# Optimization experiments

Measured on AMD Instinct MI355X. Metric: run time of the kernel, lower is better.

## Reference

```python
import jax, jax.numpy as jnp
import numpy as np

P = 2          # feature power
K = 128        # top-k neighbors
ALPHA = 1.0
BETA = 1.0
EPS = 1e-12


def _smooth_rank_l2(v):
    # v: [B, r]. torch: relu(-(v[:,None,:] - v[:,:,None])).sum(-1)
    # element [b,i,j] of diff = v[b,j] - v[b,i]; relu(-diff) = relu(v[b,i]-v[b,j])
    return jnp.sum(jax.nn.relu(v[:, :, None] - v[:, None, :]), axis=-1)  # [B, r]


def setup_inputs() -> dict:
    key = jax.random.key(0)
    k1, k2, k3 = jax.random.split(key, 3)
    B, d, N0 = 256, 2048, 7936
    return {
        "f_s": jax.random.normal(k1, (B, d), dtype=jnp.float32),
        "f_t": jax.random.normal(k2, (B, d), dtype=jnp.float32),
        "gallery": jax.random.normal(k3, (N0, d), dtype=jnp.float32),
    }


def reference(f_s, f_t, gallery):
    # pool='all': x.pow(p).view(B, -1)
    fs = f_s ** P                      # [B, d]
    ft = f_t ** P                      # [B, d]
    # statistics=True, layer 0: teacher_features = concat(existing, f_t)
    gal = jnp.concatenate([gallery, ft], axis=0)   # [N, d]

    d2 = (jnp.sum(ft * ft, axis=-1, keepdims=True)
          + jnp.sum(gal * gal, axis=-1)[None, :]
          - 2.0 * ft @ gal.T)                       # [B, N]
    tt_dist = jnp.sqrt(jnp.clip(d2, EPS, None))

    # k smallest distances (torch.sort ascending + slice [:k])
    neg_top, top_k_index = jax.lax.top_k(-tt_dist, K)
    t_value = -neg_top                               # [B, K], ascending

    # per-row re-gather of gallery and student-to-gallery distances
    gal_k = gal[top_k_index]                         # [B, K, d]
    s_d2 = (jnp.sum(fs * fs, axis=-1)[:, None]
            + jnp.sum(gal_k * gal_k, axis=-1)
            - 2.0 * jnp.einsum('bd,bkd->bk', fs, gal_k))
    s_value = jnp.sqrt(jnp.clip(s_d2, EPS, None))    # [B, K]

    main_loss = ALPHA * jnp.mean(jnp.abs(s_value[:, 0] - t_value[:, 0]))

    r = K - 1
    t_rank = _smooth_rank_l2(t_value[:, 1:])         # [B, r]
    s_rank = _smooth_rank_l2(s_value[:, 1:])         # [B, r]
    extra_loss = BETA * jnp.mean(jnp.linalg.norm(t_rank - s_rank, axis=1)) / r

    return main_loss + extra_loss
```

## Files before the change

### kernel.cpp

```cpp
#include <hip/hip_runtime.h>
#include <hip/hip_bf16.h>

#define BDIM 256
#define DDIM 2048
#define NGAL 7936
#define NTOT 8192
#define TOPK 128
#define EPSC 1e-12f

typedef __attribute__((ext_vector_type(8))) short bf16x8;
typedef __attribute__((ext_vector_type(4))) float f32x4;
typedef unsigned long long u64;

__device__ __forceinline__ short bfr(float x) {
  unsigned u = __float_as_uint(x);
  unsigned r = (u + 0x7FFFu + ((u >> 16) & 1u)) >> 16;
  return (short)r;
}

__global__ __launch_bounds__(256) void k_prep_gal(
    const float* __restrict__ f_t, const float* __restrict__ f_s,
    const float* __restrict__ gallery, short* __restrict__ Abf,
    short* __restrict__ Bbf, float* __restrict__ normA,
    float* __restrict__ galnorm) {
  int bx = blockIdx.x, t = threadIdx.x;
  int lane = t & 63, wv = t >> 6;
  if (bx < NGAL / 4) {
    int row = bx * 4 + wv;
    const float4* g4 = (const float4*)(gallery + (size_t)row * DDIM);
    float s = 0.f;
    for (int i = lane; i < DDIM / 4; i += 64) {
      float4 v = g4[i];
      *(short4*)&Bbf[(size_t)row * DDIM + i * 4] =
          make_short4(bfr(v.x), bfr(v.y), bfr(v.z), bfr(v.w));
      s += v.x * v.x + v.y * v.y + v.z * v.z + v.w * v.w;
    }
    for (int off = 32; off; off >>= 1) s += __shfl_xor(s, off);
    if (lane == 0) galnorm[row] = s;
    return;
  }
  int b = bx - NGAL / 4;
  const float4* t4 = (const float4*)(f_t + (size_t)b * DDIM);
  const float4* s4 = (const float4*)(f_s + (size_t)b * DDIM);
  float st = 0.f, ss = 0.f;
  for (int i = t; i < DDIM / 4; i += 256) {
    float4 v = t4[i];
    float4 q = make_float4(v.x * v.x, v.y * v.y, v.z * v.z, v.w * v.w);
    short4 qb = make_short4(bfr(q.x), bfr(q.y), bfr(q.z), bfr(q.w));
    *(short4*)&Abf[(size_t)b * DDIM + i * 4] = qb;
    *(short4*)&Bbf[(size_t)(NGAL + b) * DDIM + i * 4] = qb;
    st += q.x * q.x + q.y * q.y + q.z * q.z + q.w * q.w;
    float4 u_ = s4[i];
    float4 r = make_float4(u_.x * u_.x, u_.y * u_.y, u_.z * u_.z, u_.w * u_.w);
    *(short4*)&Abf[(size_t)(BDIM + b) * DDIM + i * 4] =
        make_short4(bfr(r.x), bfr(r.y), bfr(r.z), bfr(r.w));
    ss += r.x * r.x + r.y * r.y + r.z * r.z + r.w * r.w;
  }
  for (int off = 32; off; off >>= 1) {
    st += __shfl_xor(st, off);
    ss += __shfl_xor(ss, off);
  }
  __shared__ float red[8];
  if (lane == 0) { red[wv] = st; red[4 + wv] = ss; }
  __syncthreads();
  if (t == 0) {
    float a = red[0] + red[1] + red[2] + red[3];
    float c = red[4] + red[5] + red[6] + red[7];
    normA[b] = a;
    galnorm[NGAL + b] = a;
    normA[BDIM + b] = c;
  }
}

__global__ __launch_bounds__(256) void k_gemm(
    const short* __restrict__ Abf, const short* __restrict__ Bbf,
    const float* __restrict__ normA, const float* __restrict__ galnorm,
    float* __restrict__ d2) {
  __shared__ short S[2][12288];
  int t = threadIdx.x;
  int n0 = blockIdx.x * 128, m0 = blockIdx.y * 64;
  int lane = t & 63, wid = t >> 6;
  int wm = wid >> 1, wn = wid & 1;

  const short* gb[6];
  int lof[6];
#pragma unroll
  for (int q = 0; q < 6; ++q) {
    int c = t + q * 256;
    int r, j;
    const short* base;
    if (c < 512) {
      r = c >> 3; j = c & 7;
      base = Abf + (size_t)(m0 + r) * DDIM;
    } else {
      int cb = c - 512;
      r = cb >> 3; j = cb & 7;
      base = Bbf + (size_t)(n0 + r) * DDIM;
    }
    gb[q] = base + ((j * 8) ^ ((r & 7) << 3));
    lof[q] = c * 8;
  }

  int fr = lane & 15, fk = (lane >> 4) * 8;
  int axor = (fr & 7) << 3;
  f32x4 acc[2][4] = {};

#define STAGE(buf, kt)                                                       \
  {                                                                          \
    _Pragma("unroll") for (int q = 0; q < 6; ++q)                            \
        __builtin_amdgcn_global_load_lds(                                    \
            (const __attribute__((address_space(1))) void*)(gb[q] + (kt)),   \
            (__attribute__((address_space(3))) void*)(&S[buf][lof[q]]), 16,  \
            0, 0);                                                           \
  }

  STAGE(0, 0);
  __syncthreads();
  int cur = 0;
  for (int it = 0; it < DDIM / 64; ++it) {
    if (it + 1 < DDIM / 64) STAGE(cur ^ 1, (it + 1) * 64);
#pragma unroll
    for (int ks = 0; ks < 2; ++ks) {
      int ko = (ks * 32 + fk) ^ axor;
      bf16x8 av[2], bv[4];
#pragma unroll
      for (int mi = 0; mi < 2; ++mi)
        av[mi] = *(const bf16x8*)&S[cur][(wm * 32 + mi * 16 + fr) * 64 + ko];
#pragma unroll
      for (int ni = 0; ni < 4; ++ni)
        bv[ni] =
            *(const bf16x8*)&S[cur][4096 + (wn * 64 + ni * 16 + fr) * 64 + ko];
#pragma unroll
      for (int mi = 0; mi < 2; ++mi)
#pragma unroll
        for (int ni = 0; ni < 4; ++ni)
          acc[mi][ni] = __builtin_amdgcn_mfma_f32_16x16x32_bf16(
              av[mi], bv[ni], acc[mi][ni], 0, 0, 0);
    }
    __syncthreads();
    cur ^= 1;
  }
  int rrow = (lane >> 4) * 4;
#pragma unroll
  for (int mi = 0; mi < 2; ++mi) {
#pragma unroll
    for (int r = 0; r < 4; ++r) {
      int m = m0 + wm * 32 + mi * 16 + rrow + r;
      float nm = normA[m];
#pragma unroll
      for (int ni = 0; ni < 4; ++ni) {
        int n = n0 + wn * 64 + ni * 16 + fr;
        float v = nm + galnorm[n] - 2.0f * acc[mi][ni][r];
        v = fmaxf(v, EPSC);
        if (m < BDIM && n == NGAL + m) v = EPSC;
        d2[(size_t)m * NTOT + n] = v;
      }
    }
  }
#undef STAGE
}

__global__ __launch_bounds__(256) void k_part(
    const float* __restrict__ d2, u64* __restrict__ cand) {
  __shared__ unsigned rowu[2048];
  __shared__ unsigned hist[2][2048];
  __shared__ unsigned wsum[4];
  __shared__ u64 s_pref;
  __shared__ unsigned s_kneed, s_cnt;
  int c = blockIdx.x, b = blockIdx.y, t = threadIdx.x;
  int lane = t & 63, w = t >> 6;
  const uint4* src = (const uint4*)(d2 + (size_t)b * NTOT + c * 2048);
  ((uint4*)rowu)[t] = src[t];
  ((uint4*)rowu)[t + 256] = src[t + 256];
  if (t == 0) { s_pref = 0; s_kneed = TOPK; s_cnt = 0; }
#pragma unroll 1
  for (int p = 0; p < 4; ++p) {
    int sh = 33 - 11 * p;
    for (int i = t; i < 4096; i += 256) (&hist[0][0])[i] = 0;
    __syncthreads();
    u64 pref = s_pref;
    unsigned kn = s_kneed;
#pragma unroll
    for (int s = 0; s < 8; ++s) {
      int i = t + s * 256;
      u64 key = ((u64)rowu[i] << 11) | (unsigned)i;
      if ((key >> (sh + 11)) == pref) {
        unsigned bin = (unsigned)(key >> sh) & 2047u;
        unsigned slot = ((bin & 7u) << 8) | (bin >> 3);
        atomicAdd(&hist[w & 1][slot], 1u);
      }
    }
    __syncthreads();
    unsigned ls = 0;
#pragma unroll
    for (int q = 0; q < 8; ++q)
      ls += hist[0][q * 256 + t] + hist[1][q * 256 + t];
    unsigned incl = ls;
    for (int off = 1; off < 64; off <<= 1) {
      unsigned x = __shfl_up(incl, off);
      if (lane >= off) incl += x;
    }
    if (lane == 63) wsum[w] = incl;
    __syncthreads();
    unsigned woff = 0;
    for (int ww = 0; ww < w; ++ww) woff += wsum[ww];
    incl += woff;
    unsigned excl = incl - ls;
    if (excl < kn && kn <= incl) {
      unsigned re = excl, binj = 0;
      for (int q = 0; q < 8; ++q) {
        unsigned h = hist[0][q * 256 + t] + hist[1][q * 256 + t];
        if (kn <= re + h) { binj = ((unsigned)t << 3) | (unsigned)q; break; }
        re += h;
      }
      s_pref = (pref << 11) | binj;
      s_kneed = kn - re;
    }
    __syncthreads();
  }
  u64 kstar = s_pref;
  u64* dst = cand + ((size_t)b * 4 + c) * TOPK;
#pragma unroll 1
  for (int s = 0; s < 8; ++s) {
    int i = t + s * 256;
    unsigned u = rowu[i];
    u64 key = ((u64)u << 11) | (unsigned)i;
    bool pred = (key <= kstar);
    u64 mask = __ballot(pred);
    unsigned base;
    if (lane == 0) base = atomicAdd(&s_cnt, (unsigned)__popcll(mask));
    base = (unsigned)__shfl((int)base, 0);
    if (pred) {
      unsigned pos = base + (unsigned)__popcll(mask & ((1ull << lane) - 1));
      dst[pos] = ((u64)u << 13) | (unsigned)(c * 2048 + i);
    }
  }
}

__global__ __launch_bounds__(256) void k_mloss(
    const u64* __restrict__ cand, const float* __restrict__ d2,
    float* __restrict__ out) {
  __shared__ u64 sk[512];
  __shared__ float tvs[TOPK], svs[TOPK], red[2];
  int b = blockIdx.x, t = threadIdx.x;
  u64 k0 = cand[(size_t)b * 512 + t];
  u64 k1 = cand[(size_t)b * 512 + 256 + t];
  sk[t] = k0;
  sk[t + 256] = k1;
  __syncthreads();
  int r0 = 0, r1 = 0;
  for (int j = 0; j < 512; ++j) {
    u64 kj = sk[j];
    r0 += (kj < k0);
    r1 += (kj < k1);
  }
  const float* srow = d2 + (size_t)(BDIM + b) * NTOT;
  if (r0 < TOPK) {
    tvs[r0] = sqrtf(__uint_as_float((unsigned)(k0 >> 13)));
    svs[r0] = sqrtf(srow[(unsigned)(k0 & 8191u)]);
  }
  if (r1 < TOPK) {
    tvs[r1] = sqrtf(__uint_as_float((unsigned)(k1 >> 13)));
    svs[r1] = sqrtf(srow[(unsigned)(k1 & 8191u)]);
  }
  __syncthreads();
  float val = 0.f;
  if (t >= 1 && t < TOPK) {
    float tv = tvs[t], sv = svs[t];
    float tr = 0.f, sr = 0.f;
    for (int j = 0; j < TOPK; ++j) {
      tr += fmaxf(tv - tvs[j], 0.f);
      sr += fmaxf(sv - svs[j], 0.f);
    }
    tr -= fmaxf(tv - tvs[0], 0.f);
    sr -= fmaxf(sv - svs[0], 0.f);
    float d = tr - sr;
    val = d * d;
  }
  int lane = t & 63, w = t >> 6;
  for (int off = 1; off < 64; off <<= 1) val += __shfl_xor(val, off);
  if (lane == 0) red[w] = val;
  __syncthreads();
  if (t == 0) {
    float sum = red[0] + red[1];
    float contrib = (1.f / 256.f) * fabsf(svs[0] - tvs[0]) +
                    (1.f / (127.f * 256.f)) * sqrtf(sum);
    atomicAdd(out, contrib);
  }
}

extern "C" void kernel_launch(void* const* d_in, const int* in_sizes, int n_in,
                              void* d_out, int out_size, void* d_ws,
                              size_t ws_size, hipStream_t stream) {
  const float* f_s = (const float*)d_in[0];
  const float* f_t = (const float*)d_in[1];
  const float* gallery = (const float*)d_in[2];
  float* out = (float*)d_out;

  float* d2 = (float*)d_ws;
  short* Abf = (short*)(d2 + (size_t)512 * NTOT);
  short* Bbf = Abf + (size_t)512 * DDIM;
  float* normA = (float*)(Bbf + (size_t)NTOT * DDIM);
  float* galnorm = normA + 512;
  u64* cand = (u64*)(galnorm + NTOT);

  hipMemsetAsync(d_out, 0, sizeof(float), stream);

  k_prep_gal<<<NGAL / 4 + BDIM, 256, 0, stream>>>(f_t, f_s, gallery, Abf, Bbf,
                                                  normA, galnorm);
  k_gemm<<<dim3(NTOT / 128, 512 / 64), 256, 0, stream>>>(Abf, Bbf, normA,
                                                         galnorm, d2);
  k_part<<<dim3(4, BDIM), 256, 0, stream>>>(d2, cand);
  k_mloss<<<BDIM, 256, 0, stream>>>(cand, d2, out);
}
```

Baseline: 163.2 us.

## Swizzle GEMM tiles per XCD and cut radix-select passes to three

The GEMM launch becomes a 1D grid whose block index is remapped so that consecutive blocks on each XCD share N tiles and all 8 M tiles. This is meant to raise L2 reuse of the gallery operand. The top-k partition kernel now radix-selects on the 32-bit value alone in three passes (11/11/10 bits) instead of four passes on a 43-bit value+index key, and breaks ties among equal values with a small index-rank pass. This removes one histogram pass and the 64-bit key arithmetic, at the cost of extra tie-handling logic that caps equal-value collection at 256 entries.

```diff
diff --git a/kernel.cpp b/kernel.cpp
--- a/kernel.cpp
+++ b/kernel.cpp
@@ -78,7 +78,11 @@
     float* __restrict__ d2) {
   __shared__ short S[2][12288];
   int t = threadIdx.x;
-  int n0 = blockIdx.x * 128, m0 = blockIdx.y * 64;
+  int swz = blockIdx.x;
+  int xcd = swz & 7, p = swz >> 3;
+  int nt = xcd * 8 + (p >> 3);
+  int mt = p & 7;
+  int n0 = nt * 128, m0 = mt * 64;
   int lane = t & 63, wid = t >> 6;
   int wm = wid >> 1, wn = wid & 1;
 
@@ -165,27 +169,32 @@
   __shared__ unsigned rowu[2048];
   __shared__ unsigned hist[2][2048];
   __shared__ unsigned wsum[4];
-  __shared__ u64 s_pref;
-  __shared__ unsigned s_kneed, s_cnt;
+  __shared__ unsigned s_pref, s_kneed, s_cnt, s_eqcnt;
+  __shared__ unsigned short eqidx[256];
   int c = blockIdx.x, b = blockIdx.y, t = threadIdx.x;
   int lane = t & 63, w = t >> 6;
   const uint4* src = (const uint4*)(d2 + (size_t)b * NTOT + c * 2048);
   ((uint4*)rowu)[t] = src[t];
   ((uint4*)rowu)[t + 256] = src[t + 256];
-  if (t == 0) { s_pref = 0; s_kneed = TOPK; s_cnt = 0; }
+  if (t == 0) { s_pref = 0; s_kneed = TOPK; s_cnt = 0; s_eqcnt = 0; }
 #pragma unroll 1
-  for (int p = 0; p < 4; ++p) {
-    int sh = 33 - 11 * p;
-    for (int i = t; i < 4096; i += 256) (&hist[0][0])[i] = 0;
-    __syncthreads();
-    u64 pref = s_pref;
-    unsigned kn = s_kneed;
+  for (int p = 0; p < 3; ++p) {
+    int sh = (p == 0) ? 21 : (p == 1) ? 10 : 0;
+    uint4 z4 = make_uint4(0, 0, 0, 0);
+    ((uint4*)&hist[0][0])[t] = z4;
+    ((uint4*)&hist[0][0])[t + 256] = z4;
+    ((uint4*)&hist[0][0])[t + 512] = z4;
+    ((uint4*)&hist[0][0])[t + 768] = z4;
+    __syncthreads();
+    unsigned pref = s_pref, kn = s_kneed;
+    int sh_hi = (p == 1) ? 21 : 10;
+    unsigned bmask = (p == 2) ? 1023u : 2047u;
 #pragma unroll
     for (int s = 0; s < 8; ++s) {
-      int i = t + s * 256;
-      u64 key = ((u64)rowu[i] << 11) | (unsigned)i;
-      if ((key >> (sh + 11)) == pref) {
-        unsigned bin = (unsigned)(key >> sh) & 2047u;
+      unsigned u = rowu[t + s * 256];
+      bool sel = (p == 0) || ((u >> sh_hi) == pref);
+      if (sel) {
+        unsigned bin = (u >> sh) & bmask;
         unsigned slot = ((bin & 7u) << 8) | (bin >> 3);
         atomicAdd(&hist[w & 1][slot], 1u);
       }
@@ -213,26 +222,43 @@
         if (kn <= re + h) { binj = ((unsigned)t << 3) | (unsigned)q; break; }
         re += h;
       }
-      s_pref = (pref << 11) | binj;
+      unsigned bits = (p == 2) ? 10u : 11u;
+      s_pref = (pref << bits) | binj;
       s_kneed = kn - re;
     }
     __syncthreads();
   }
-  u64 kstar = s_pref;
+  unsigned vstar = s_pref;
+  unsigned kneed = s_kneed;
   u64* dst = cand + ((size_t)b * 4 + c) * TOPK;
 #pragma unroll 1
   for (int s = 0; s < 8; ++s) {
     int i = t + s * 256;
     unsigned u = rowu[i];
-    u64 key = ((u64)u << 11) | (unsigned)i;
-    bool pred = (key <= kstar);
-    u64 mask = __ballot(pred);
-    unsigned base;
-    if (lane == 0) base = atomicAdd(&s_cnt, (unsigned)__popcll(mask));
-    base = (unsigned)__shfl((int)base, 0);
-    if (pred) {
-      unsigned pos = base + (unsigned)__popcll(mask & ((1ull << lane) - 1));
+    bool lt = (u < vstar);
+    u64 mlt = __ballot(lt);
+    unsigned basep;
+    if (lane == 0) basep = atomicAdd(&s_cnt, (unsigned)__popcll(mlt));
+    basep = (unsigned)__shfl((int)basep, 0);
+    if (lt) {
+      unsigned pos = basep + (unsigned)__popcll(mlt & ((1ull << lane) - 1));
       dst[pos] = ((u64)u << 13) | (unsigned)(c * 2048 + i);
+    }
+    if (u == vstar) {
+      unsigned e = atomicAdd(&s_eqcnt, 1u);
+      if (e < 256) eqidx[e] = (unsigned short)i;
+    }
+  }
+  __syncthreads();
+  unsigned ce = s_eqcnt;
+  if (ce > 256) ce = 256;
+  if (t < (int)ce) {
+    unsigned short my = eqidx[t];
+    unsigned rank = 0;
+    for (unsigned j = 0; j < ce; ++j) rank += (eqidx[j] < my);
+    if (rank < kneed) {
+      unsigned pos = atomicAdd(&s_cnt, 1u);
+      dst[pos] = ((u64)vstar << 13) | (unsigned)(c * 2048 + (int)my);
     }
   }
 }
@@ -308,8 +334,7 @@
 
   k_prep_gal<<<NGAL / 4 + BDIM, 256, 0, stream>>>(f_t, f_s, gallery, Abf, Bbf,
                                                   normA, galnorm);
-  k_gemm<<<dim3(NTOT / 128, 512 / 64), 256, 0, stream>>>(Abf, Bbf, normA,
-                                                         galnorm, d2);
+  k_gemm<<<512, 256, 0, stream>>>(Abf, Bbf, normA, galnorm, d2);
   k_part<<<dim3(4, BDIM), 256, 0, stream>>>(d2, cand);
   k_mloss<<<BDIM, 256, 0, stream>>>(cand, d2, out);
 }
```

New measurement: 159.7 us. -2.2%, faster.
